# Performance work log

Hardware: AMD Instinct MI355X
Metric: run time of the kernel (lower is better)

## Reference

```python
import jax, jax.numpy as jnp
import numpy as np

N = 30000
E = 600000
IN = 64
HID = 128
EPS = 1e-5
HEADS_PER_LAYER = (4, 4, 1)


def _bn(x, g, b):
    # eval-mode BatchNorm: running_mean=0, running_var=1
    return x * (g / np.sqrt(1.0 + EPS)) + b


def _segment_softmax(e, dst, n):
    m = jax.ops.segment_max(e, dst, num_segments=n)
    ex = jnp.exp(e - m[dst])
    s = jax.ops.segment_sum(ex, dst, num_segments=n)
    return ex / (s[dst] + 1e-16)


def _gcn_conv(x, w, b, src, dst, norm, n):
    m = (x @ w)[src] * norm[:, None]            # [E+N, HID]
    return jax.ops.segment_sum(m, dst, num_segments=n) + b


def _gat_conv(x, w, a_src, a_dst, b, src, dst, n, heads):
    C = HID // heads
    xh = (x @ w).reshape(n, heads, C)
    asrc = (xh * a_src.reshape(heads, C)).sum(-1)   # [N, heads]
    adst = (xh * a_dst.reshape(heads, C)).sum(-1)
    e = jax.nn.leaky_relu(asrc[src] + adst[dst], 0.2)  # [E+N, heads]
    alpha = _segment_softmax(e, dst, n)
    out = jax.ops.segment_sum(xh[src] * alpha[:, :, None], dst, num_segments=n)
    return out.reshape(n, HID) + b


def _forward(x, gcn_in_w, gcn_in_b, gcn_res_w, gcn_res_b, gcn_w, gcn_b,
             gcn_bn_g, gcn_bn_b, gcn_c1w, gcn_c1b, gcn_c2w, gcn_c2b,
             gcn_c3w, gcn_c3b, gat_in_w, gat_in_b, gat_w, gat_asrc,
             gat_adst, gat_b, gat_bn_g, gat_bn_b, feat_imp, gat_c1w,
             gat_c1b, gat_cbn_g, gat_cbn_b, gat_c2w, gat_c2b, gat_c3w,
             gat_c3b, fin_w, fin_b, fin_bn_g, fin_bn_b, fin2_w, fin2_b,
             edge_index):
    n = x.shape[0]
    loop = jnp.arange(n, dtype=edge_index.dtype)
    src = jnp.concatenate([edge_index[0], loop])  # add self-loops
    dst = jnp.concatenate([edge_index[1], loop])
    # GCN symmetric normalization (with self-loops)
    deg = jax.ops.segment_sum(jnp.ones_like(dst, dtype=x.dtype), dst, num_segments=n)
    dis = jnp.where(deg > 0, jax.lax.rsqrt(jnp.maximum(deg, 1.0)), 0.0)
    norm = dis[src] * dis[dst]

    # ---- GCN branch (eval: dropout = identity, self-attn skipped since N>5000) ----
    xp = x @ gcn_in_w + gcn_in_b
    res = x @ gcn_res_w + gcn_res_b
    for i in range(3):
        xn = _gcn_conv(xp, gcn_w[i], gcn_b[i], src, dst, norm, n)
        xn = jax.nn.relu(_bn(xn, gcn_bn_g[i], gcn_bn_b[i]))
        if i % 2 == 1:
            xp = xn + res
            res = xp
        else:
            xp = xn
    h = jax.nn.relu(xp @ gcn_c1w + gcn_c1b)
    h = jax.nn.relu(h @ gcn_c2w + gcn_c2b)
    gcn_out = h @ gcn_c3w + gcn_c3b

    # ---- GAT branch ----
    xg = x @ gat_in_w + gat_in_b
    for i in range(3):
        xg = _gat_conv(xg, gat_w[i], gat_asrc[i], gat_adst[i], gat_b[i],
                       src, dst, n, HEADS_PER_LAYER[i])
        xg = jax.nn.elu(_bn(xg, gat_bn_g[i], gat_bn_b[i]))
    xg = xg * feat_imp
    h = jax.nn.relu(xg @ gat_c1w + gat_c1b)
    h = _bn(h, gat_cbn_g, gat_cbn_b)
    h = jax.nn.relu(h @ gat_c2w + gat_c2b)
    gat_out = h @ gat_c3w + gat_c3b

    # ---- fusion: N > 10000 -> weighted blend path ----
    fused = 0.6 * gcn_out + 0.4 * gat_out
    h = jax.nn.relu(fused @ fin_w + fin_b)
    h = _bn(h, fin_bn_g, fin_bn_b)
    return h @ fin2_w + fin2_b  # [N, 2]


def setup_inputs() -> dict:
    key = jax.random.key(0)
    ks = iter(jax.random.split(key, 64))

    def nrm(shape, scale=1.0):
        return jax.random.normal(next(ks), shape, dtype=jnp.float32) * scale

    s_in = 1.0 / np.sqrt(IN)
    s_h = 1.0 / np.sqrt(HID)
    inp = {}
    inp['x'] = nrm((N, IN))
    inp['edge_index'] = jax.random.randint(next(ks), (2, E), 0, N, dtype=jnp.int32)
    inp['gcn_in_w'] = nrm((IN, HID), s_in); inp['gcn_in_b'] = nrm((HID,), 0.01)
    inp['gcn_res_w'] = nrm((IN, HID), s_in); inp['gcn_res_b'] = nrm((HID,), 0.01)
    inp['gcn_w'] = nrm((3, HID, HID), s_h); inp['gcn_b'] = nrm((3, HID), 0.01)
    inp['gcn_bn_g'] = 1.0 + nrm((3, HID), 0.1); inp['gcn_bn_b'] = nrm((3, HID), 0.1)
    inp['gcn_c1w'] = nrm((HID, 64), s_h); inp['gcn_c1b'] = nrm((64,), 0.01)
    inp['gcn_c2w'] = nrm((64, 32), 0.125); inp['gcn_c2b'] = nrm((32,), 0.01)
    inp['gcn_c3w'] = nrm((32, HID), 0.18); inp['gcn_c3b'] = nrm((HID,), 0.01)
    inp['gat_in_w'] = nrm((IN, HID), s_in); inp['gat_in_b'] = nrm((HID,), 0.01)
    inp['gat_w'] = nrm((3, HID, HID), s_h)
    inp['gat_asrc'] = nrm((3, HID), s_h); inp['gat_adst'] = nrm((3, HID), s_h)
    inp['gat_b'] = nrm((3, HID), 0.01)
    inp['gat_bn_g'] = 1.0 + nrm((3, HID), 0.1); inp['gat_bn_b'] = nrm((3, HID), 0.1)
    inp['feat_imp'] = 1.0 + nrm((HID,), 0.1)
    inp['gat_c1w'] = nrm((HID, 64), s_h); inp['gat_c1b'] = nrm((64,), 0.01)
    inp['gat_cbn_g'] = 1.0 + nrm((64,), 0.1); inp['gat_cbn_b'] = nrm((64,), 0.1)
    inp['gat_c2w'] = nrm((64, 32), 0.125); inp['gat_c2b'] = nrm((32,), 0.01)
    inp['gat_c3w'] = nrm((32, HID), 0.18); inp['gat_c3b'] = nrm((HID,), 0.01)
    inp['fin_w'] = nrm((HID, 64), s_h); inp['fin_b'] = nrm((64,), 0.01)
    inp['fin_bn_g'] = 1.0 + nrm((64,), 0.1); inp['fin_bn_b'] = nrm((64,), 0.1)
    inp['fin2_w'] = nrm((64, 2), 0.125); inp['fin2_b'] = nrm((2,), 0.01)
    return inp


def reference(x, edge_index, gcn_in_w, gcn_in_b, gcn_res_w, gcn_res_b, gcn_w,
              gcn_b, gcn_bn_g, gcn_bn_b, gcn_c1w, gcn_c1b, gcn_c2w, gcn_c2b,
              gcn_c3w, gcn_c3b, gat_in_w, gat_in_b, gat_w, gat_asrc, gat_adst,
              gat_b, gat_bn_g, gat_bn_b, feat_imp, gat_c1w, gat_c1b, gat_cbn_g,
              gat_cbn_b, gat_c2w, gat_c2b, gat_c3w, gat_c3b, fin_w, fin_b,
              fin_bn_g, fin_bn_b, fin2_w, fin2_b):
    return _forward(x, gcn_in_w, gcn_in_b, gcn_res_w, gcn_res_b, gcn_w, gcn_b,
                    gcn_bn_g, gcn_bn_b, gcn_c1w, gcn_c1b, gcn_c2w, gcn_c2b,
                    gcn_c3w, gcn_c3b, gat_in_w, gat_in_b, gat_w, gat_asrc,
                    gat_adst, gat_b, gat_bn_g, gat_bn_b, feat_imp, gat_c1w,
                    gat_c1b, gat_cbn_g, gat_cbn_b, gat_c2w, gat_c2b, gat_c3w,
                    gat_c3b, fin_w, fin_b, fin_bn_g, fin_bn_b, fin2_w, fin2_b,
                    edge_index)
```

## Files before the change

kernel.cpp:

```cpp
#include <hip/hip_runtime.h>
#include <hip/hip_fp16.h>

#define RSQ_BN 0.9999950000374997f

typedef _Float16 f16x8 __attribute__((ext_vector_type(8)));
typedef float f32x4 __attribute__((ext_vector_type(4)));

union H8u { uint4 u4; __half h[8]; };
union H4u { uint2 u2; __half h[4]; };

__device__ __forceinline__ float leaky02(float x) { return x > 0.f ? x : 0.2f * x; }

__device__ __forceinline__ float4 ld4(const float* p) {
    return *reinterpret_cast<const float4*>(p);
}
__device__ __forceinline__ void ld8(float* d, const float* p) {
    float4 u = ld4(p), v = ld4(p + 4);
    d[0] = u.x; d[1] = u.y; d[2] = u.z; d[3] = u.w;
    d[4] = v.x; d[5] = v.y; d[6] = v.z; d[7] = v.w;
}


__global__ void hist_k(const int* __restrict__ edst, int* __restrict__ cnt, int E, int EN) {
    int i = blockIdx.x * 256 + threadIdx.x;
    if (i >= EN) return;
    int d = (i < E) ? edst[i] : (i - E);
    atomicAdd(&cnt[d], 1);
}

__global__ __launch_bounds__(256)
void scanA_k(const int* __restrict__ cnt, int* __restrict__ rowptr,
             int* __restrict__ bsum, int n) {
    __shared__ int sh[256];
    int t = threadIdx.x;
    int i = blockIdx.x * 256 + t;
    int v = (i < n) ? cnt[i] : 0;
    sh[t] = v;
    __syncthreads();
#pragma unroll
    for (int off = 1; off < 256; off <<= 1) {
        int u = 0;
        if (t >= off) u = sh[t - off];
        __syncthreads();
        sh[t] += u;
        __syncthreads();
    }
    if (i < n) rowptr[i] = sh[t] - v;
    if (t == 255) bsum[blockIdx.x] = sh[255];
}

__global__ __launch_bounds__(256)
void scanB_k(int* __restrict__ bsum, int nb) {
    __shared__ int sh[256];
    int t = threadIdx.x;
    int v = (t < nb) ? bsum[t] : 0;
    sh[t] = v;
    __syncthreads();
#pragma unroll
    for (int off = 1; off < 256; off <<= 1) {
        int u = 0;
        if (t >= off) u = sh[t - off];
        __syncthreads();
        sh[t] += u;
        __syncthreads();
    }
    if (t < nb) bsum[t] = sh[t] - v;
}

__global__ __launch_bounds__(256)
void scanC_k(const int* __restrict__ cnt, const int* __restrict__ bsum,
             int* __restrict__ rowptr, int* __restrict__ cursor,
             float* __restrict__ dis, int n, int EN) {
    int i = blockIdx.x * 256 + threadIdx.x;
    if (i < n) {
        int r = rowptr[i] + bsum[blockIdx.x];
        rowptr[i] = r;
        cursor[i] = r;
        dis[i] = rsqrtf((float)cnt[i]);
    }
    if (i == 0) rowptr[n] = EN;
}

__global__ void scatter_k(const int* __restrict__ esrc, const int* __restrict__ edst,
                          int* __restrict__ cursor, int* __restrict__ colidx, int E, int EN) {
    int i = blockIdx.x * 256 + threadIdx.x;
    if (i >= EN) return;
    int s, d;
    if (i < E) { s = esrc[i]; d = edst[i]; }
    else       { s = i - E; d = s; }
    int pos = atomicAdd(&cursor[d], 1);
    colidx[pos] = s;
}


__device__ __forceinline__ float pd0_elem(const float* __restrict__ gat_w,
                                          const float* __restrict__ gat_asrc,
                                          const float* __restrict__ gat_adst,
                                          int t, int col) {
    float p = 0.f;
    if (col < 4) {
        const float* w = gat_w + (size_t)t * 128 + col * 32;
        const float* av = gat_asrc + col * 32;
        for (int c2 = 0; c2 < 32; ++c2) p += w[c2] * av[c2];
    } else if (col >= 8 && col < 12) {
        int hh2 = col - 8;
        const float* w = gat_w + (size_t)t * 128 + hh2 * 32;
        const float* av = gat_adst + hh2 * 32;
        for (int c2 = 0; c2 < 32; ++c2) p += w[c2] * av[c2];
    }
    return p;
}

__global__ void wtx_all_k(const float* __restrict__ gcn_in_w, const float* __restrict__ gcn_res_w,
                          const float* __restrict__ gat_in_w,
                          const float* __restrict__ gcn_w, const float* __restrict__ gat_w,
                          const float* __restrict__ gcn_c1w, const float* __restrict__ gat_c1w,
                          const float* __restrict__ gcn_c3w, const float* __restrict__ gat_c3w,
                          const float* __restrict__ fin_w,
                          const float* __restrict__ gcn_c2w, const float* __restrict__ gat_c2w,
                          const float* __restrict__ gat_asrc, const float* __restrict__ gat_adst,
                          const float* __restrict__ gcn_in_b, const float* __restrict__ gat_in_b,
                          __half* __restrict__ WTin, __half* __restrict__ WTg,
                          __half* __restrict__ WTa, __half* __restrict__ WTc1,
                          __half* __restrict__ WTc3, __half* __restrict__ WTfin,
                          __half* __restrict__ WTc2, __half* __restrict__ WTd,
                          __half* __restrict__ Mg0, __half* __restrict__ Ma0,
                          __half* __restrict__ Da, float* __restrict__ cg0,
                          float* __restrict__ ca0, float* __restrict__ oa) {
    int idx = blockIdx.x * 256 + threadIdx.x;
    const float* src;
    __half* dst;
    int K, M, o;
    if (idx < 24576) {
        int mi = idx >> 13; o = idx & 8191;
        src = mi == 0 ? gcn_in_w : (mi == 1 ? gcn_res_w : gat_in_w);
        dst = WTin + mi * 8192; K = 64; M = 128;
    } else if (idx < 73728) {
        int r = idx - 24576; int mi = r >> 14; o = r & 16383;
        src = gcn_w + mi * 16384; dst = WTg + mi * 16384; K = 128; M = 128;
    } else if (idx < 122880) {
        int r = idx - 73728; int mi = r >> 14; o = r & 16383;
        src = gat_w + mi * 16384; dst = WTa + mi * 16384; K = 128; M = 128;
    } else if (idx < 139264) {
        int r = idx - 122880; int mi = r >> 13; o = r & 8191;
        src = mi ? gat_c1w : gcn_c1w; dst = WTc1 + mi * 8192; K = 128; M = 64;
    } else if (idx < 147456) {
        int r = idx - 139264; int mi = r >> 12; o = r & 4095;
        src = mi ? gat_c3w : gcn_c3w; dst = WTc3 + mi * 4096; K = 32; M = 128;
    } else if (idx < 155648) {
        o = idx - 147456; src = fin_w; dst = WTfin; K = 128; M = 64;
    } else if (idx < 159744) {
        int r = idx - 155648; int mi = r >> 11; o = r & 2047;
        src = mi ? gat_c2w : gcn_c2w; dst = WTc2 + mi * 2048; K = 64; M = 32;
    } else if (idx < 165888) {
        int r = idx - 159744;
        int layer = r >> 11; o = r & 2047;
        int j = o & 7, lane = (o >> 3) & 63, k32 = o >> 9;
        int col = lane & 15, quad = lane >> 4;
        int k = k32 * 32 + quad * 8 + j;
        int hh = (layer < 2) ? 4 : 1;
        int C = 128 / hh;
        float v = 0.f;
        if (col < hh) {
            const float* w = gat_w + (size_t)(layer * 128 + k) * 128 + col * C;
            const float* av = gat_asrc + layer * 128 + col * C;
            for (int c2 = 0; c2 < C; ++c2) v += w[c2] * av[c2];
        } else if (col >= 8 && col < 8 + hh) {
            int hthis = col - 8;
            const float* w = gat_w + (size_t)(layer * 128 + k) * 128 + hthis * C;
            const float* av = gat_adst + layer * 128 + hthis * C;
            for (int c2 = 0; c2 < C; ++c2) v += w[c2] * av[c2];
        }
        WTd[(size_t)layer * 2048 + o] = (__half)v;
        return;
    } else if (idx < 183296) {
        int r = idx - 165888;
        bool isA = r >= 8192;
        o = r & 8191;
        int j = o & 7, lane = (o >> 3) & 63, rr = o >> 9;
        int ct = rr >> 1, k32 = rr & 1;
        int m = lane & 15, quad = lane >> 4;
        int k = k32 * 32 + quad * 8 + j;
        int col = ct * 16 + m;
        const float* inw = isA ? gat_in_w : gcn_in_w;
        const float* lw  = isA ? gat_w : gcn_w;
        float v = 0.f;
        for (int t = 0; t < 128; ++t) v += inw[k * 128 + t] * lw[(size_t)t * 128 + col];
        (isA ? Ma0 : Mg0)[o] = (__half)v;
        return;
    } else if (idx < 184320) {
        o = idx - 183296;
        int j = o & 7, lane = (o >> 3) & 63, k32 = o >> 9;
        int col = lane & 15, quad = lane >> 4;
        int k = k32 * 32 + quad * 8 + j;
        float v = 0.f;
        if (col < 4 || (col >= 8 && col < 12)) {
            for (int t = 0; t < 128; ++t)
                v += gat_in_w[k * 128 + t] * pd0_elem(gat_w, gat_asrc, gat_adst, t, col);
        }
        Da[o] = (__half)v;
        return;
    } else if (idx < 184448) {
        int col = idx - 184320;
        float v = 0.f;
        for (int t = 0; t < 128; ++t) v += gcn_in_b[t] * gcn_w[(size_t)t * 128 + col];
        cg0[col] = v;
        return;
    } else if (idx < 184576) {
        int col = idx - 184448;
        float v = 0.f;
        for (int t = 0; t < 128; ++t) v += gat_in_b[t] * gat_w[(size_t)t * 128 + col];
        ca0[col] = v;
        return;
    } else if (idx < 184592) {
        int col = idx - 184576;
        float v = 0.f;
        if (col < 4 || (col >= 8 && col < 12)) {
            for (int t = 0; t < 128; ++t)
                v += gat_in_b[t] * pd0_elem(gat_w, gat_asrc, gat_adst, t, col);
        }
        oa[col] = v;
        return;
    } else return;
    int j = o & 7, lane = (o >> 3) & 63, r = o >> 9;
    int KD32 = K >> 5;
    int ct = r / KD32, k32 = r - ct * KD32;
    int m = lane & 15, quad = lane >> 4;
    int k = k32 * 32 + quad * 8 + j;
    int mcol = ct * 16 + m;
    dst[o] = (__half)src[k * M + mcol];
}


__device__ __forceinline__ f16x8 mk_af(const float* xr, int kb) {
    float4 v0 = ld4(xr + kb), v1 = ld4(xr + kb + 4);
    f16x8 af;
    af[0] = (_Float16)v0.x; af[1] = (_Float16)v0.y;
    af[2] = (_Float16)v0.z; af[3] = (_Float16)v0.w;
    af[4] = (_Float16)v1.x; af[5] = (_Float16)v1.y;
    af[6] = (_Float16)v1.z; af[7] = (_Float16)v1.w;
    return af;
}


__global__ __launch_bounds__(256)
void dual0_mfma_k(const float* __restrict__ X,
                  const __half* __restrict__ Mg0, const __half* __restrict__ Wres,
                  const float* __restrict__ resb,
                  const __half* __restrict__ Ma0, const __half* __restrict__ Da,
                  const float* __restrict__ cg0, const float* __restrict__ ca0,
                  const float* __restrict__ oa,
                  const float* __restrict__ dis,
                  __half* __restrict__ Yg, __half* __restrict__ Rout,
                  __half* __restrict__ Ya,
                  float* __restrict__ avp, float* __restrict__ bvp,
                  int hh, int n, int gper) {
    bool gat = blockIdx.x >= gper;
    int blk = gat ? blockIdx.x - gper : blockIdx.x;
    int wave = threadIdx.x >> 6, lane = threadIdx.x & 63;
    int m = lane & 15, quad = lane >> 4;
    int row0 = blk * 64 + wave * 16;
    int arow = min(row0 + m, n - 1);
    const float* xr = X + (size_t)arow * 64;
    f16x8 xf0 = mk_af(xr, quad * 8);
    f16x8 xf1 = mk_af(xr, 32 + quad * 8);
    int row = row0 + m;
    f32x4 acc[8];
    if (!gat) {
#pragma unroll
        for (int ct = 0; ct < 8; ++ct) acc[ct] = (f32x4){0.f, 0.f, 0.f, 0.f};
#pragma unroll
        for (int ct = 0; ct < 8; ++ct) {
            f16x8 b0 = *reinterpret_cast<const f16x8*>(Mg0 + ((ct * 2 + 0) << 9) + (lane << 3));
            f16x8 b1 = *reinterpret_cast<const f16x8*>(Mg0 + ((ct * 2 + 1) << 9) + (lane << 3));
            acc[ct] = __builtin_amdgcn_mfma_f32_16x16x32_f16(b0, xf0, acc[ct], 0, 0, 0);
            acc[ct] = __builtin_amdgcn_mfma_f32_16x16x32_f16(b1, xf1, acc[ct], 0, 0, 0);
        }
        if (row < n) {
            float dv = dis[row];
#pragma unroll
            for (int ct = 0; ct < 8; ++ct) {
                int col = ct * 16 + quad * 4;
                float4 cb = ld4(cg0 + col);
                H4u w;
                w.h[0] = (__half)((acc[ct][0] + cb.x) * dv);
                w.h[1] = (__half)((acc[ct][1] + cb.y) * dv);
                w.h[2] = (__half)((acc[ct][2] + cb.z) * dv);
                w.h[3] = (__half)((acc[ct][3] + cb.w) * dv);
                *reinterpret_cast<uint2*>(Yg + (size_t)row * 128 + col) = w.u2;
            }
        }
#pragma unroll
        for (int ct = 0; ct < 8; ++ct) acc[ct] = (f32x4){0.f, 0.f, 0.f, 0.f};
#pragma unroll
        for (int ct = 0; ct < 8; ++ct) {
            f16x8 b0 = *reinterpret_cast<const f16x8*>(Wres + ((ct * 2 + 0) << 9) + (lane << 3));
            f16x8 b1 = *reinterpret_cast<const f16x8*>(Wres + ((ct * 2 + 1) << 9) + (lane << 3));
            acc[ct] = __builtin_amdgcn_mfma_f32_16x16x32_f16(b0, xf0, acc[ct], 0, 0, 0);
            acc[ct] = __builtin_amdgcn_mfma_f32_16x16x32_f16(b1, xf1, acc[ct], 0, 0, 0);
        }
        if (row < n) {
#pragma unroll
            for (int ct = 0; ct < 8; ++ct) {
                int col = ct * 16 + quad * 4;
                float4 cb = ld4(resb + col);
                H4u w;
                w.h[0] = (__half)(acc[ct][0] + cb.x);
                w.h[1] = (__half)(acc[ct][1] + cb.y);
                w.h[2] = (__half)(acc[ct][2] + cb.z);
                w.h[3] = (__half)(acc[ct][3] + cb.w);
                *reinterpret_cast<uint2*>(Rout + (size_t)row * 128 + col) = w.u2;
            }
        }
    } else {
        f32x4 accd = (f32x4){0.f, 0.f, 0.f, 0.f};
#pragma unroll
        for (int ct = 0; ct < 8; ++ct) acc[ct] = (f32x4){0.f, 0.f, 0.f, 0.f};
#pragma unroll
        for (int ct = 0; ct < 8; ++ct) {
            f16x8 b0 = *reinterpret_cast<const f16x8*>(Ma0 + ((ct * 2 + 0) << 9) + (lane << 3));
            f16x8 b1 = *reinterpret_cast<const f16x8*>(Ma0 + ((ct * 2 + 1) << 9) + (lane << 3));
            acc[ct] = __builtin_amdgcn_mfma_f32_16x16x32_f16(b0, xf0, acc[ct], 0, 0, 0);
            acc[ct] = __builtin_amdgcn_mfma_f32_16x16x32_f16(b1, xf1, acc[ct], 0, 0, 0);
        }
        {
            f16x8 d0 = *reinterpret_cast<const f16x8*>(Da + (0 << 9) + (lane << 3));
            f16x8 d1 = *reinterpret_cast<const f16x8*>(Da + (1 << 9) + (lane << 3));
            accd = __builtin_amdgcn_mfma_f32_16x16x32_f16(d0, xf0, accd, 0, 0, 0);
            accd = __builtin_amdgcn_mfma_f32_16x16x32_f16(d1, xf1, accd, 0, 0, 0);
        }
        if (row < n) {
#pragma unroll
            for (int ct = 0; ct < 8; ++ct) {
                int col = ct * 16 + quad * 4;
                float4 cb = ld4(ca0 + col);
                H4u w;
                w.h[0] = (__half)(acc[ct][0] + cb.x);
                w.h[1] = (__half)(acc[ct][1] + cb.y);
                w.h[2] = (__half)(acc[ct][2] + cb.z);
                w.h[3] = (__half)(acc[ct][3] + cb.w);
                *reinterpret_cast<uint2*>(Ya + (size_t)row * 128 + col) = w.u2;
            }
            if (quad == 0) {
#pragma unroll
                for (int reg = 0; reg < 4; ++reg)
                    if (reg < hh) avp[row * hh + reg] = accd[reg] + oa[reg];
            } else if (quad == 2) {
#pragma unroll
                for (int reg = 0; reg < 4; ++reg)
                    if (reg < hh) bvp[row * hh + reg] = accd[reg] + oa[8 + reg];
            }
        }
    }
}


__global__ __launch_bounds__(256)
void dual128_mfma_k(const __half* __restrict__ Xg, const __half* __restrict__ WTg,
                    __half* __restrict__ Yg,
                    const __half* __restrict__ Xa, const __half* __restrict__ WTa,
                    __half* __restrict__ Ya,
                    const float* __restrict__ dis,
                    const __half* __restrict__ WTd,
                    float* __restrict__ avp, float* __restrict__ bvp,
                    int hh, int n, int gper) {
    bool gat = blockIdx.x >= gper;
    int blk = gat ? blockIdx.x - gper : blockIdx.x;
    const __half* X = gat ? Xa : Xg;
    const __half* WT = gat ? WTa : WTg;
    __half* Y = gat ? Ya : Yg;
    int wave = threadIdx.x >> 6;
    int lane = threadIdx.x & 63;
    int m = lane & 15, quad = lane >> 4;
    int row0 = blk * 64 + wave * 16;
    int arow = min(row0 + m, n - 1);
    const __half* xr = X + (size_t)arow * 128;
    f32x4 acc[8];
#pragma unroll
    for (int ct = 0; ct < 8; ++ct) acc[ct] = (f32x4){0.f, 0.f, 0.f, 0.f};
    int row = row0 + m;
    if (!gat) {
#pragma unroll
        for (int k32 = 0; k32 < 4; ++k32) {
            int kb = k32 * 32 + quad * 8;
            f16x8 af = *reinterpret_cast<const f16x8*>(xr + kb);
#pragma unroll
            for (int ct = 0; ct < 8; ++ct) {
                f16x8 bf = *reinterpret_cast<const f16x8*>(WT + ((ct * 4 + k32) << 9) + (lane << 3));
                acc[ct] = __builtin_amdgcn_mfma_f32_16x16x32_f16(bf, af, acc[ct], 0, 0, 0);
            }
        }
        if (row < n) {
            float dv = dis[row];
#pragma unroll
            for (int ct = 0; ct < 8; ++ct) {
                int col = ct * 16 + quad * 4;
                H4u w;
                w.h[0] = (__half)(acc[ct][0] * dv);
                w.h[1] = (__half)(acc[ct][1] * dv);
                w.h[2] = (__half)(acc[ct][2] * dv);
                w.h[3] = (__half)(acc[ct][3] * dv);
                *reinterpret_cast<uint2*>(Y + (size_t)row * 128 + col) = w.u2;
            }
        }
    } else {
        f32x4 accd = (f32x4){0.f, 0.f, 0.f, 0.f};
#pragma unroll
        for (int k32 = 0; k32 < 4; ++k32) {
            int kb = k32 * 32 + quad * 8;
            f16x8 af = *reinterpret_cast<const f16x8*>(xr + kb);
#pragma unroll
            for (int ct = 0; ct < 8; ++ct) {
                f16x8 bf = *reinterpret_cast<const f16x8*>(WT + ((ct * 4 + k32) << 9) + (lane << 3));
                acc[ct] = __builtin_amdgcn_mfma_f32_16x16x32_f16(bf, af, acc[ct], 0, 0, 0);
            }
            f16x8 bd = *reinterpret_cast<const f16x8*>(WTd + (k32 << 9) + (lane << 3));
            accd = __builtin_amdgcn_mfma_f32_16x16x32_f16(bd, af, accd, 0, 0, 0);
        }
        if (row < n) {
#pragma unroll
            for (int ct = 0; ct < 8; ++ct) {
                int col = ct * 16 + quad * 4;
                H4u w;
                w.h[0] = (__half)acc[ct][0];
                w.h[1] = (__half)acc[ct][1];
                w.h[2] = (__half)acc[ct][2];
                w.h[3] = (__half)acc[ct][3];
                *reinterpret_cast<uint2*>(Y + (size_t)row * 128 + col) = w.u2;
            }
            if (quad == 0) {
#pragma unroll
                for (int reg = 0; reg < 4; ++reg)
                    if (reg < hh) avp[row * hh + reg] = accd[reg];
            } else if (quad == 2) {
#pragma unroll
                for (int reg = 0; reg < 4; ++reg)
                    if (reg < hh) bvp[row * hh + reg] = accd[reg];
            }
        }
    }
}


__global__ __launch_bounds__(256)
void fused_gather_k(const int* __restrict__ rowptr, const int* __restrict__ colidx,
                    const float* __restrict__ dis,
                    const __half* __restrict__ Tg, const float* __restrict__ gbias,
                    const float* __restrict__ gbng, const float* __restrict__ gbnb,
                    const __half* __restrict__ res, __half* __restrict__ Yg,
                    const __half* __restrict__ Ta, const float* __restrict__ avp,
                    const float* __restrict__ bvp, const float* __restrict__ abias,
                    const float* __restrict__ abng, const float* __restrict__ abnb,
                    const float* __restrict__ fimp, __half* __restrict__ Ya,
                    int n, int hh, int log2C) {
    int idx = blockIdx.x * 256 + threadIdx.x;
    int i = idx >> 4;
    if (i >= n) return;
    int c = (idx & 15) * 8;
    int h = c >> log2C;
    float ad = bvp[i * hh + h];
    int p0 = rowptr[i], p1 = rowptr[i + 1];
    float g[8], a[8];
#pragma unroll
    for (int t = 0; t < 8; ++t) { g[t] = 0.f; a[t] = 0.f; }
    float m = -3.0e38f, s = 0.f;

    int ng = (p1 - p0 + 3) >> 2;
    int p = p0;
    int sx[4]; float av[4], vm[4];
#pragma unroll
    for (int j = 0; j < 4; ++j) {
        int q = p0 + j;
        vm[j] = (q < p1) ? 1.f : 0.f;
        sx[j] = colidx[min(q, p1 - 1)];
    }
#pragma unroll
    for (int j = 0; j < 4; ++j) av[j] = avp[sx[j] * hh + h];

    for (int gi = 0; gi < ng; ++gi) {
        uint4 qg[4], qa[4];
#pragma unroll
        for (int j = 0; j < 4; ++j)
            qg[j] = *reinterpret_cast<const uint4*>(Tg + (size_t)sx[j] * 128 + c);
#pragma unroll
        for (int j = 0; j < 4; ++j)
            qa[j] = *reinterpret_cast<const uint4*>(Ta + (size_t)sx[j] * 128 + c);
        int pn = p + 4;
        int sn[4]; float avn[4], vmn[4];
#pragma unroll
        for (int j = 0; j < 4; ++j) {
            int q = pn + j;
            vmn[j] = (q < p1) ? 1.f : 0.f;
            sn[j] = colidx[min(max(q, p0), p1 - 1)];
        }
#pragma unroll
        for (int j = 0; j < 4; ++j) avn[j] = avp[sn[j] * hh + h];
        float e0 = vm[0] > 0.f ? leaky02(av[0] + ad) : -3.0e38f;
        float e1 = vm[1] > 0.f ? leaky02(av[1] + ad) : -3.0e38f;
        float e2 = vm[2] > 0.f ? leaky02(av[2] + ad) : -3.0e38f;
        float e3 = vm[3] > 0.f ? leaky02(av[3] + ad) : -3.0e38f;
        float mc = fmaxf(fmaxf(e0, e1), fmaxf(e2, e3));
        float mn = fmaxf(m, mc);
        float scale = __expf(m - mn);
        float w0 = __expf(e0 - mn), w1 = __expf(e1 - mn);
        float w2 = __expf(e2 - mn), w3 = __expf(e3 - mn);
        s = s * scale + (w0 + w1 + w2 + w3);
        m = mn;
        {
            H8u k0, k1, k2, k3;
            k0.u4 = qg[0]; k1.u4 = qg[1]; k2.u4 = qg[2]; k3.u4 = qg[3];
#pragma unroll
            for (int t = 0; t < 8; ++t) {
                float v = g[t];
                v = fmaf(__half2float(k0.h[t]), vm[0], v);
                v = fmaf(__half2float(k1.h[t]), vm[1], v);
                v = fmaf(__half2float(k2.h[t]), vm[2], v);
                v = fmaf(__half2float(k3.h[t]), vm[3], v);
                g[t] = v;
            }
        }
        {
            H8u k0, k1, k2, k3;
            k0.u4 = qa[0]; k1.u4 = qa[1]; k2.u4 = qa[2]; k3.u4 = qa[3];
#pragma unroll
            for (int t = 0; t < 8; ++t) {
                float v = a[t] * scale;
                v = fmaf(__half2float(k0.h[t]), w0, v);
                v = fmaf(__half2float(k1.h[t]), w1, v);
                v = fmaf(__half2float(k2.h[t]), w2, v);
                v = fmaf(__half2float(k3.h[t]), w3, v);
                a[t] = v;
            }
        }
        p = pn;
#pragma unroll
        for (int j = 0; j < 4; ++j) { sx[j] = sn[j]; av[j] = avn[j]; vm[j] = vmn[j]; }
    }

    {
        float di = dis[i];
        float bb[8], gg[8], nb[8];
        ld8(bb, gbias + c); ld8(gg, gbng + c); ld8(nb, gbnb + c);
        float o[8];
#pragma unroll
        for (int t = 0; t < 8; ++t) {
            float v = g[t] * di + bb[t];
            o[t] = fmaxf(v * (gg[t] * RSQ_BN) + nb[t], 0.f);
        }
        if (res) {
            H8u rr;
            rr.u4 = *reinterpret_cast<const uint4*>(res + (size_t)i * 128 + c);
#pragma unroll
            for (int t = 0; t < 8; ++t) o[t] += __half2float(rr.h[t]);
        }
        H8u w;
#pragma unroll
        for (int t = 0; t < 8; ++t) w.h[t] = (__half)o[t];
        *reinterpret_cast<uint4*>(Yg + (size_t)i * 128 + c) = w.u4;
    }
    {
        float si = 1.f / (s + 1e-16f);
        float bb[8], gg[8], nb[8];
        ld8(bb, abias + c); ld8(gg, abng + c); ld8(nb, abnb + c);
        float o[8];
#pragma unroll
        for (int t = 0; t < 8; ++t) {
            float v = a[t] * si + bb[t];
            v = v * (gg[t] * RSQ_BN) + nb[t];
            o[t] = v > 0.f ? v : expm1f(v);
        }
        if (fimp) {
            float ff[8]; ld8(ff, fimp + c);
#pragma unroll
            for (int t = 0; t < 8; ++t) o[t] *= ff[t];
        }
        H8u w;
#pragma unroll
        for (int t = 0; t < 8; ++t) w.h[t] = (__half)o[t];
        *reinterpret_cast<uint4*>(Ya + (size_t)i * 128 + c) = w.u4;
    }
}


__global__ __launch_bounds__(256)
void fused_tail_k(const __half* __restrict__ Xg, const __half* __restrict__ Xa,
                  const __half* __restrict__ WTc1,
                  const float* __restrict__ c1bg, const float* __restrict__ c1ba,
                  const float* __restrict__ cbng, const float* __restrict__ cbnb,
                  const __half* __restrict__ WTc2,
                  const float* __restrict__ c2bg, const float* __restrict__ c2ba,
                  const __half* __restrict__ WTc3,
                  const float* __restrict__ c3bg, const float* __restrict__ c3ba,
                  const __half* __restrict__ WTfin, const float* __restrict__ finb,
                  const float* __restrict__ fbng, const float* __restrict__ fbnb,
                  const float* __restrict__ w2, const float* __restrict__ b2,
                  float* __restrict__ out, int n) {
    __shared__ alignas(16) __half h1s[2][64][88];
    __shared__ alignas(16) __half h2s[2][64][56];
    __shared__ alignas(16) __half Fs[64][152];
    int wave = threadIdx.x >> 6, lane = threadIdx.x & 63;
    int m = lane & 15, quad = lane >> 4;
    int row0 = blockIdx.x * 64 + wave * 16;
    int lr0 = wave * 16;
    int arow = min(row0 + m, n - 1);

#pragma unroll
    for (int br = 0; br < 2; ++br) {
        const __half* xr = (br ? Xa : Xg) + (size_t)arow * 128;
        const __half* WT = WTc1 + br * 8192;
        f32x4 acc[4];
#pragma unroll
        for (int ct = 0; ct < 4; ++ct) acc[ct] = (f32x4){0.f, 0.f, 0.f, 0.f};
#pragma unroll
        for (int k32 = 0; k32 < 4; ++k32) {
            int kb = k32 * 32 + quad * 8;
            f16x8 af = *reinterpret_cast<const f16x8*>(xr + kb);
#pragma unroll
            for (int ct = 0; ct < 4; ++ct) {
                f16x8 bf = *reinterpret_cast<const f16x8*>(WT + ((ct * 4 + k32) << 9) + (lane << 3));
                acc[ct] = __builtin_amdgcn_mfma_f32_16x16x32_f16(af, bf, acc[ct], 0, 0, 0);
            }
        }
        const float* bi = br ? c1ba : c1bg;
#pragma unroll
        for (int ct = 0; ct < 4; ++ct) {
            int col = ct * 16 + m;
            float cb = bi[col];
            float cg = br ? cbng[col] * RSQ_BN : 1.f;
            float cbb = br ? cbnb[col] : 0.f;
#pragma unroll
            for (int reg = 0; reg < 4; ++reg) {
                float v = fmaxf(acc[ct][reg] + cb, 0.f) * cg + cbb;
                h1s[br][lr0 + quad * 4 + reg][col] = (__half)v;
            }
        }
    }
    __syncthreads();
#pragma unroll
    for (int br = 0; br < 2; ++br) {
        f32x4 acc[2];
        acc[0] = (f32x4){0.f, 0.f, 0.f, 0.f};
        acc[1] = (f32x4){0.f, 0.f, 0.f, 0.f};
        const __half* WT = WTc2 + br * 2048;
#pragma unroll
        for (int k32 = 0; k32 < 2; ++k32) {
            int kb = k32 * 32 + quad * 8;
            f16x8 af = *reinterpret_cast<const f16x8*>(&h1s[br][lr0 + m][kb]);
#pragma unroll
            for (int ct = 0; ct < 2; ++ct) {
                f16x8 bf = *reinterpret_cast<const f16x8*>(WT + ((ct * 2 + k32) << 9) + (lane << 3));
                acc[ct] = __builtin_amdgcn_mfma_f32_16x16x32_f16(af, bf, acc[ct], 0, 0, 0);
            }
        }
        const float* bi = br ? c2ba : c2bg;
#pragma unroll
        for (int ct = 0; ct < 2; ++ct) {
            int col = ct * 16 + m;
            float cb = bi[col];
#pragma unroll
            for (int reg = 0; reg < 4; ++reg) {
                float v = fmaxf(acc[ct][reg] + cb, 0.f);
                h2s[br][lr0 + quad * 4 + reg][col] = (__half)v;
            }
        }
    }
    __syncthreads();
    {
        f32x4 ag[8], aa[8];
#pragma unroll
        for (int ct = 0; ct < 8; ++ct) {
            ag[ct] = (f32x4){0.f, 0.f, 0.f, 0.f};
            aa[ct] = (f32x4){0.f, 0.f, 0.f, 0.f};
        }
        int kb = quad * 8;
        f16x8 afg = *reinterpret_cast<const f16x8*>(&h2s[0][lr0 + m][kb]);
        f16x8 afa = *reinterpret_cast<const f16x8*>(&h2s[1][lr0 + m][kb]);
#pragma unroll
        for (int ct = 0; ct < 8; ++ct) {
            f16x8 bfg = *reinterpret_cast<const f16x8*>(WTc3 + (ct << 9) + (lane << 3));
            f16x8 bfa = *reinterpret_cast<const f16x8*>(WTc3 + 4096 + (ct << 9) + (lane << 3));
            ag[ct] = __builtin_amdgcn_mfma_f32_16x16x32_f16(afg, bfg, ag[ct], 0, 0, 0);
            aa[ct] = __builtin_amdgcn_mfma_f32_16x16x32_f16(afa, bfa, aa[ct], 0, 0, 0);
        }
#pragma unroll
        for (int ct = 0; ct < 8; ++ct) {
            int col = ct * 16 + m;
            float cb = 0.6f * c3bg[col] + 0.4f * c3ba[col];
#pragma unroll
            for (int reg = 0; reg < 4; ++reg) {
                float v = 0.6f * ag[ct][reg] + 0.4f * aa[ct][reg] + cb;
                Fs[lr0 + quad * 4 + reg][col] = (__half)v;
            }
        }
    }
    __syncthreads();
    {
        f32x4 acc[4];
#pragma unroll
        for (int ct = 0; ct < 4; ++ct) acc[ct] = (f32x4){0.f, 0.f, 0.f, 0.f};
#pragma unroll
        for (int k32 = 0; k32 < 4; ++k32) {
            int kb = k32 * 32 + quad * 8;
            f16x8 af = *reinterpret_cast<const f16x8*>(&Fs[lr0 + m][kb]);
#pragma unroll
            for (int ct = 0; ct < 4; ++ct) {
                f16x8 bf = *reinterpret_cast<const f16x8*>(WTfin + ((ct * 4 + k32) << 9) + (lane << 3));
                acc[ct] = __builtin_amdgcn_mfma_f32_16x16x32_f16(af, bf, acc[ct], 0, 0, 0);
            }
        }
        float p0[4] = {0.f, 0.f, 0.f, 0.f}, p1[4] = {0.f, 0.f, 0.f, 0.f};
#pragma unroll
        for (int ct = 0; ct < 4; ++ct) {
            int col = ct * 16 + m;
            float cb = finb[col];
            float cg = fbng[col] * RSQ_BN;
            float cbb = fbnb[col];
            float w20 = w2[2 * col], w21 = w2[2 * col + 1];
#pragma unroll
            for (int reg = 0; reg < 4; ++reg) {
                float v = fmaxf(acc[ct][reg] + cb, 0.f) * cg + cbb;
                p0[reg] += v * w20;
                p1[reg] += v * w21;
            }
        }
        for (int off = 1; off < 16; off <<= 1) {
#pragma unroll
            for (int reg = 0; reg < 4; ++reg) {
                p0[reg] += __shfl_xor(p0[reg], off);
                p1[reg] += __shfl_xor(p1[reg], off);
            }
        }
        if (m == 0) {
#pragma unroll
            for (int reg = 0; reg < 4; ++reg) {
                int row = row0 + quad * 4 + reg;
                if (row < n) {
                    out[row * 2] = p0[reg] + b2[0];
                    out[row * 2 + 1] = p1[reg] + b2[1];
                }
            }
        }
    }
}


static inline int cdiv(int a, int b) { return (a + b - 1) / b; }

extern "C" void kernel_launch(void* const* d_in, const int* in_sizes, int n_in,
                              void* d_out, int out_size, void* d_ws, size_t ws_size,
                              hipStream_t stream) {
    const float* x       = (const float*)d_in[0];
    const int*   ei      = (const int*)d_in[1];
    const float* gcn_in_w = (const float*)d_in[2];
    const float* gcn_in_b = (const float*)d_in[3];
    const float* gcn_res_w = (const float*)d_in[4];
    const float* gcn_res_b = (const float*)d_in[5];
    const float* gcn_w   = (const float*)d_in[6];
    const float* gcn_b   = (const float*)d_in[7];
    const float* gcn_bn_g = (const float*)d_in[8];
    const float* gcn_bn_b = (const float*)d_in[9];
    const float* gcn_c1w = (const float*)d_in[10];
    const float* gcn_c1b = (const float*)d_in[11];
    const float* gcn_c2w = (const float*)d_in[12];
    const float* gcn_c2b = (const float*)d_in[13];
    const float* gcn_c3w = (const float*)d_in[14];
    const float* gcn_c3b = (const float*)d_in[15];
    const float* gat_in_w = (const float*)d_in[16];
    const float* gat_in_b = (const float*)d_in[17];
    const float* gat_w   = (const float*)d_in[18];
    const float* gat_asrc = (const float*)d_in[19];
    const float* gat_adst = (const float*)d_in[20];
    const float* gat_b   = (const float*)d_in[21];
    const float* gat_bn_g = (const float*)d_in[22];
    const float* gat_bn_b = (const float*)d_in[23];
    const float* feat_imp = (const float*)d_in[24];
    const float* gat_c1w = (const float*)d_in[25];
    const float* gat_c1b = (const float*)d_in[26];
    const float* gat_cbn_g = (const float*)d_in[27];
    const float* gat_cbn_b = (const float*)d_in[28];
    const float* gat_c2w = (const float*)d_in[29];
    const float* gat_c2b = (const float*)d_in[30];
    const float* gat_c3w = (const float*)d_in[31];
    const float* gat_c3b = (const float*)d_in[32];
    const float* fin_w   = (const float*)d_in[33];
    const float* fin_b   = (const float*)d_in[34];
    const float* fin_bn_g = (const float*)d_in[35];
    const float* fin_bn_b = (const float*)d_in[36];
    const float* fin2_w  = (const float*)d_in[37];
    const float* fin2_b  = (const float*)d_in[38];

    const int N = in_sizes[0] / 64;
    const int E = in_sizes[1] / 2;
    const int EN = E + N;
    const int* esrc = ei;
    const int* edst = ei + E;

    char* wp = (char*)d_ws;
    auto alloc = [&](size_t bytes) -> void* {
        void* p = (void*)wp;
        wp += (bytes + 255) & ~(size_t)255;
        return p;
    };
    int* cnt    = (int*)alloc((size_t)N * 4);
    int* rowptr = (int*)alloc((size_t)(N + 1) * 4);
    int* cursor = (int*)alloc((size_t)N * 4);
    int* bsum   = (int*)alloc((size_t)256 * 4);
    int* colidx = (int*)alloc((size_t)EN * 4);
    float* dis  = (float*)alloc((size_t)N * 4);
    __half* A   = (__half*)alloc((size_t)N * 128 * 2);
    __half* B   = (__half*)alloc((size_t)N * 128 * 2);
    __half* G   = (__half*)alloc((size_t)N * 128 * 2);
    __half* H   = (__half*)alloc((size_t)N * 128 * 2);
    __half* R   = (__half*)alloc((size_t)N * 128 * 2);
    __half* Th1 = (__half*)alloc((size_t)N * 128 * 2);
    __half* Th2 = (__half*)alloc((size_t)N * 128 * 2);
    float* avv  = (float*)alloc((size_t)N * 4 * 4);
    float* bvv  = (float*)alloc((size_t)N * 4 * 4);
    __half* WTin = (__half*)alloc((size_t)3 * 8192 * 2);
    __half* WTg  = (__half*)alloc((size_t)3 * 16384 * 2);
    __half* WTa  = (__half*)alloc((size_t)3 * 16384 * 2);
    __half* WTc1 = (__half*)alloc((size_t)2 * 8192 * 2);
    __half* WTc3 = (__half*)alloc((size_t)2 * 4096 * 2);
    __half* WTfin = (__half*)alloc((size_t)8192 * 2);
    __half* WTc2 = (__half*)alloc((size_t)2 * 2048 * 2);
    __half* WTd  = (__half*)alloc((size_t)3 * 2048 * 2);
    __half* Mg0  = (__half*)alloc((size_t)8192 * 2);
    __half* Ma0  = (__half*)alloc((size_t)8192 * 2);
    __half* Da   = (__half*)alloc((size_t)1024 * 2);
    float* cg0   = (float*)alloc((size_t)128 * 4);
    float* ca0   = (float*)alloc((size_t)128 * 4);
    float* oa    = (float*)alloc((size_t)16 * 4);

    const int nScanB = cdiv(N, 256);
    hipMemsetAsync(cnt, 0, (size_t)N * 4, stream);
    hist_k<<<cdiv(EN, 256), 256, 0, stream>>>(edst, cnt, E, EN);
    scanA_k<<<nScanB, 256, 0, stream>>>(cnt, rowptr, bsum, N);
    scanB_k<<<1, 256, 0, stream>>>(bsum, nScanB);
    scanC_k<<<nScanB, 256, 0, stream>>>(cnt, bsum, rowptr, cursor, dis, N, EN);
    scatter_k<<<cdiv(EN, 256), 256, 0, stream>>>(esrc, edst, cursor, colidx, E, EN);
    wtx_all_k<<<721, 256, 0, stream>>>(gcn_in_w, gcn_res_w, gat_in_w, gcn_w, gat_w,
                                       gcn_c1w, gat_c1w, gcn_c3w, gat_c3w, fin_w,
                                       gcn_c2w, gat_c2w, gat_asrc, gat_adst,
                                       gcn_in_b, gat_in_b,
                                       WTin, WTg, WTa, WTc1, WTc3, WTfin, WTc2, WTd,
                                       Mg0, Ma0, Da, cg0, ca0, oa);

    const int g64r = cdiv(N, 64);
    const int gG   = cdiv(N, 16);

    dual0_mfma_k<<<2 * g64r, 256, 0, stream>>>(x, Mg0, WTin + 8192, gcn_res_b,
                                               Ma0, Da, cg0, ca0, oa, dis,
                                               Th1, R, Th2, avv, bvv, 4, N, g64r);
    fused_gather_k<<<gG, 256, 0, stream>>>(rowptr, colidx, dis,
                                           Th1, gcn_b, gcn_bn_g, gcn_bn_b, nullptr, A,
                                           Th2, avv, bvv, gat_b, gat_bn_g, gat_bn_b,
                                           nullptr, G, N, 4, 5);
    dual128_mfma_k<<<2 * g64r, 256, 0, stream>>>(A, WTg + 16384, Th1,
                                                 G, WTa + 16384, Th2, dis,
                                                 WTd + 2048, avv, bvv, 4, N, g64r);
    fused_gather_k<<<gG, 256, 0, stream>>>(rowptr, colidx, dis,
                                           Th1, gcn_b + 128, gcn_bn_g + 128, gcn_bn_b + 128,
                                           R, B,
                                           Th2, avv, bvv, gat_b + 128, gat_bn_g + 128,
                                           gat_bn_b + 128, nullptr, H, N, 4, 5);
    dual128_mfma_k<<<2 * g64r, 256, 0, stream>>>(B, WTg + 32768, Th1,
                                                 H, WTa + 32768, Th2, dis,
                                                 WTd + 4096, avv, bvv, 1, N, g64r);
    fused_gather_k<<<gG, 256, 0, stream>>>(rowptr, colidx, dis,
                                           Th1, gcn_b + 256, gcn_bn_g + 256, gcn_bn_b + 256,
                                           nullptr, A,
                                           Th2, avv, bvv, gat_b + 256, gat_bn_g + 256,
                                           gat_bn_b + 256, feat_imp, G, N, 1, 7);

    fused_tail_k<<<g64r, 256, 0, stream>>>(A, G,
                                           WTc1, gcn_c1b, gat_c1b, gat_cbn_g, gat_cbn_b,
                                           WTc2, gcn_c2b, gat_c2b,
                                           WTc3, gcn_c3b, gat_c3b,
                                           WTfin, fin_b, fin_bn_g, fin_bn_b,
                                           fin2_w, fin2_b, (float*)d_out, N);
}
```

Before: 435.7 us.

## Split fused gather threads across GCN/GAT tables and column halves

The fused gather kernel now assigns each thread a single table (GCN or GAT) and an 8-column chunk within one 64-column half, so each node is covered by two blocks with twice as many threads. Each thread keeps one accumulator array instead of two and issues half as many feature loads per edge. This halves per-thread register pressure and doubles the parallelism for latency hiding. In exchange, the colidx, rowptr and attention-score loads and the softmax arithmetic are repeated across more threads, and GCN threads perform redundant softmax work.

```diff
diff --git a/kernel.cpp b/kernel.cpp
--- a/kernel.cpp
+++ b/kernel.cpp
@@ -453,16 +453,19 @@
                     const float* __restrict__ abng, const float* __restrict__ abnb,
                     const float* __restrict__ fimp, __half* __restrict__ Ya,
                     int n, int hh, int log2C) {
-    int idx = blockIdx.x * 256 + threadIdx.x;
-    int i = idx >> 4;
+    int slice = blockIdx.x & 1;
+    int i = (blockIdx.x >> 1) * 16 + (threadIdx.x >> 4);
     if (i >= n) return;
-    int c = (idx & 15) * 8;
+    int k = threadIdx.x & 15;
+    int tbl = k >> 3;
+    int c = slice * 64 + (k & 7) * 8;
     int h = c >> log2C;
-    float ad = bvp[i * hh + h];
+    const __half* T = tbl ? Ta : Tg;
+    float ad = tbl ? bvp[i * hh + h] : 0.f;
     int p0 = rowptr[i], p1 = rowptr[i + 1];
-    float g[8], a[8];
-#pragma unroll
-    for (int t = 0; t < 8; ++t) { g[t] = 0.f; a[t] = 0.f; }
+    float acc[8];
+#pragma unroll
+    for (int t = 0; t < 8; ++t) acc[t] = 0.f;
     float m = -3.0e38f, s = 0.f;
 
     int ng = (p1 - p0 + 3) >> 2;
@@ -475,16 +478,13 @@
         sx[j] = colidx[min(q, p1 - 1)];
     }
 #pragma unroll
-    for (int j = 0; j < 4; ++j) av[j] = avp[sx[j] * hh + h];
+    for (int j = 0; j < 4; ++j) av[j] = tbl ? avp[sx[j] * hh + h] : 0.f;
 
     for (int gi = 0; gi < ng; ++gi) {
-        uint4 qg[4], qa[4];
+        uint4 q4[4];
 #pragma unroll
         for (int j = 0; j < 4; ++j)
-            qg[j] = *reinterpret_cast<const uint4*>(Tg + (size_t)sx[j] * 128 + c);
-#pragma unroll
-        for (int j = 0; j < 4; ++j)
-            qa[j] = *reinterpret_cast<const uint4*>(Ta + (size_t)sx[j] * 128 + c);
+            q4[j] = *reinterpret_cast<const uint4*>(T + (size_t)sx[j] * 128 + c);
         int pn = p + 4;
         int sn[4]; float avn[4], vmn[4];
 #pragma unroll
@@ -494,7 +494,7 @@
             sn[j] = colidx[min(max(q, p0), p1 - 1)];
         }
 #pragma unroll
-        for (int j = 0; j < 4; ++j) avn[j] = avp[sn[j] * hh + h];
+        for (int j = 0; j < 4; ++j) avn[j] = tbl ? avp[sn[j] * hh + h] : 0.f;
         float e0 = vm[0] > 0.f ? leaky02(av[0] + ad) : -3.0e38f;
         float e1 = vm[1] > 0.f ? leaky02(av[1] + ad) : -3.0e38f;
         float e2 = vm[2] > 0.f ? leaky02(av[2] + ad) : -3.0e38f;
@@ -506,45 +506,35 @@
         float w2 = __expf(e2 - mn), w3 = __expf(e3 - mn);
         s = s * scale + (w0 + w1 + w2 + w3);
         m = mn;
-        {
-            H8u k0, k1, k2, k3;
-            k0.u4 = qg[0]; k1.u4 = qg[1]; k2.u4 = qg[2]; k3.u4 = qg[3];
-#pragma unroll
-            for (int t = 0; t < 8; ++t) {
-                float v = g[t];
-                v = fmaf(__half2float(k0.h[t]), vm[0], v);
-                v = fmaf(__half2float(k1.h[t]), vm[1], v);
-                v = fmaf(__half2float(k2.h[t]), vm[2], v);
-                v = fmaf(__half2float(k3.h[t]), vm[3], v);
-                g[t] = v;
-            }
-        }
-        {
-            H8u k0, k1, k2, k3;
-            k0.u4 = qa[0]; k1.u4 = qa[1]; k2.u4 = qa[2]; k3.u4 = qa[3];
-#pragma unroll
-            for (int t = 0; t < 8; ++t) {
-                float v = a[t] * scale;
-                v = fmaf(__half2float(k0.h[t]), w0, v);
-                v = fmaf(__half2float(k1.h[t]), w1, v);
-                v = fmaf(__half2float(k2.h[t]), w2, v);
-                v = fmaf(__half2float(k3.h[t]), w3, v);
-                a[t] = v;
-            }
+        float u0 = tbl ? w0 : vm[0];
+        float u1 = tbl ? w1 : vm[1];
+        float u2 = tbl ? w2 : vm[2];
+        float u3 = tbl ? w3 : vm[3];
+        float sc = tbl ? scale : 1.f;
+        H8u k0, k1, k2, k3;
+        k0.u4 = q4[0]; k1.u4 = q4[1]; k2.u4 = q4[2]; k3.u4 = q4[3];
+#pragma unroll
+        for (int t = 0; t < 8; ++t) {
+            float v = acc[t] * sc;
+            v = fmaf(__half2float(k0.h[t]), u0, v);
+            v = fmaf(__half2float(k1.h[t]), u1, v);
+            v = fmaf(__half2float(k2.h[t]), u2, v);
+            v = fmaf(__half2float(k3.h[t]), u3, v);
+            acc[t] = v;
         }
         p = pn;
 #pragma unroll
         for (int j = 0; j < 4; ++j) { sx[j] = sn[j]; av[j] = avn[j]; vm[j] = vmn[j]; }
     }
 
-    {
+    if (tbl == 0) {
         float di = dis[i];
         float bb[8], gg[8], nb[8];
         ld8(bb, gbias + c); ld8(gg, gbng + c); ld8(nb, gbnb + c);
         float o[8];
 #pragma unroll
         for (int t = 0; t < 8; ++t) {
-            float v = g[t] * di + bb[t];
+            float v = acc[t] * di + bb[t];
             o[t] = fmaxf(v * (gg[t] * RSQ_BN) + nb[t], 0.f);
         }
         if (res) {
@@ -557,15 +547,14 @@
 #pragma unroll
         for (int t = 0; t < 8; ++t) w.h[t] = (__half)o[t];
         *reinterpret_cast<uint4*>(Yg + (size_t)i * 128 + c) = w.u4;
-    }
-    {
+    } else {
         float si = 1.f / (s + 1e-16f);
         float bb[8], gg[8], nb[8];
         ld8(bb, abias + c); ld8(gg, abng + c); ld8(nb, abnb + c);
         float o[8];
 #pragma unroll
         for (int t = 0; t < 8; ++t) {
-            float v = a[t] * si + bb[t];
+            float v = acc[t] * si + bb[t];
             v = v * (gg[t] * RSQ_BN) + nb[t];
             o[t] = v > 0.f ? v : expm1f(v);
         }
@@ -846,7 +835,7 @@
                                        Mg0, Ma0, Da, cg0, ca0, oa);
 
     const int g64r = cdiv(N, 64);
-    const int gG   = cdiv(N, 16);
+    const int gG   = 2 * cdiv(N, 16);
 
     dual0_mfma_k<<<2 * g64r, 256, 0, stream>>>(x, Mg0, WTin + 8192, gcn_res_b,
                                                Ma0, Da, cg0, ca0, oa, dis,
```

Result: slower. 444.9 us (+2.1%).

## Split fused gather into separate GCN and GAT block slices

Applied to the files above, without the earlier changes.

The fused gather kernel previously had each thread accumulate both the GCN sum and the GAT softmax-weighted sum for 8 channels. Now blocks are split four ways: two slices handle the GCN half-rows and two handle the GAT half-rows, each processing 32 nodes of 8 threads per block. This lowers per-thread register pressure and raises parallelism. In exchange, the colidx and index loads are repeated across slices, and the GAT softmax statistics are recomputed in both GAT slices. Column index loads also switch to nontemporal loads.

```diff
diff --git a/kernel.cpp b/kernel.cpp
--- a/kernel.cpp
+++ b/kernel.cpp
@@ -453,119 +453,134 @@
                     const float* __restrict__ abng, const float* __restrict__ abnb,
                     const float* __restrict__ fimp, __half* __restrict__ Ya,
                     int n, int hh, int log2C) {
-    int idx = blockIdx.x * 256 + threadIdx.x;
-    int i = idx >> 4;
+    int slice = blockIdx.x & 3;
+    int i = (blockIdx.x >> 2) * 32 + (threadIdx.x >> 3);
     if (i >= n) return;
-    int c = (idx & 15) * 8;
-    int h = c >> log2C;
-    float ad = bvp[i * hh + h];
+    int c = (slice & 1) * 64 + (threadIdx.x & 7) * 8;
     int p0 = rowptr[i], p1 = rowptr[i + 1];
-    float g[8], a[8];
-#pragma unroll
-    for (int t = 0; t < 8; ++t) { g[t] = 0.f; a[t] = 0.f; }
-    float m = -3.0e38f, s = 0.f;
-
     int ng = (p1 - p0 + 3) >> 2;
-    int p = p0;
-    int sx[4]; float av[4], vm[4];
-#pragma unroll
-    for (int j = 0; j < 4; ++j) {
-        int q = p0 + j;
-        vm[j] = (q < p1) ? 1.f : 0.f;
-        sx[j] = colidx[min(q, p1 - 1)];
-    }
-#pragma unroll
-    for (int j = 0; j < 4; ++j) av[j] = avp[sx[j] * hh + h];
-
-    for (int gi = 0; gi < ng; ++gi) {
-        uint4 qg[4], qa[4];
-#pragma unroll
-        for (int j = 0; j < 4; ++j)
-            qg[j] = *reinterpret_cast<const uint4*>(Tg + (size_t)sx[j] * 128 + c);
-#pragma unroll
-        for (int j = 0; j < 4; ++j)
-            qa[j] = *reinterpret_cast<const uint4*>(Ta + (size_t)sx[j] * 128 + c);
-        int pn = p + 4;
-        int sn[4]; float avn[4], vmn[4];
+    float acc[8];
+#pragma unroll
+    for (int t = 0; t < 8; ++t) acc[t] = 0.f;
+
+    if (slice < 2) {
+        int p = p0;
+        int sx[4]; float vm[4];
 #pragma unroll
         for (int j = 0; j < 4; ++j) {
-            int q = pn + j;
-            vmn[j] = (q < p1) ? 1.f : 0.f;
-            sn[j] = colidx[min(max(q, p0), p1 - 1)];
-        }
-#pragma unroll
-        for (int j = 0; j < 4; ++j) avn[j] = avp[sn[j] * hh + h];
-        float e0 = vm[0] > 0.f ? leaky02(av[0] + ad) : -3.0e38f;
-        float e1 = vm[1] > 0.f ? leaky02(av[1] + ad) : -3.0e38f;
-        float e2 = vm[2] > 0.f ? leaky02(av[2] + ad) : -3.0e38f;
-        float e3 = vm[3] > 0.f ? leaky02(av[3] + ad) : -3.0e38f;
-        float mc = fmaxf(fmaxf(e0, e1), fmaxf(e2, e3));
-        float mn = fmaxf(m, mc);
-        float scale = __expf(m - mn);
-        float w0 = __expf(e0 - mn), w1 = __expf(e1 - mn);
-        float w2 = __expf(e2 - mn), w3 = __expf(e3 - mn);
-        s = s * scale + (w0 + w1 + w2 + w3);
-        m = mn;
-        {
+            int q = p0 + j;
+            vm[j] = (q < p1) ? 1.f : 0.f;
+            sx[j] = __builtin_nontemporal_load(colidx + min(q, p1 - 1));
+        }
+        for (int gi = 0; gi < ng; ++gi) {
+            uint4 q4[4];
+#pragma unroll
+            for (int j = 0; j < 4; ++j)
+                q4[j] = *reinterpret_cast<const uint4*>(Tg + (size_t)sx[j] * 128 + c);
+            int pn = p + 4;
+            int sn[4]; float vmn[4];
+#pragma unroll
+            for (int j = 0; j < 4; ++j) {
+                int q = pn + j;
+                vmn[j] = (q < p1) ? 1.f : 0.f;
+                sn[j] = __builtin_nontemporal_load(colidx + min(max(q, p0), p1 - 1));
+            }
             H8u k0, k1, k2, k3;
-            k0.u4 = qg[0]; k1.u4 = qg[1]; k2.u4 = qg[2]; k3.u4 = qg[3];
+            k0.u4 = q4[0]; k1.u4 = q4[1]; k2.u4 = q4[2]; k3.u4 = q4[3];
 #pragma unroll
             for (int t = 0; t < 8; ++t) {
-                float v = g[t];
+                float v = acc[t];
                 v = fmaf(__half2float(k0.h[t]), vm[0], v);
                 v = fmaf(__half2float(k1.h[t]), vm[1], v);
                 v = fmaf(__half2float(k2.h[t]), vm[2], v);
                 v = fmaf(__half2float(k3.h[t]), vm[3], v);
-                g[t] = v;
-            }
-        }
-        {
+                acc[t] = v;
+            }
+            p = pn;
+#pragma unroll
+            for (int j = 0; j < 4; ++j) { sx[j] = sn[j]; vm[j] = vmn[j]; }
+        }
+        float di = dis[i];
+        float bb[8], gg[8], nb[8];
+        ld8(bb, gbias + c); ld8(gg, gbng + c); ld8(nb, gbnb + c);
+        float o[8];
+#pragma unroll
+        for (int t = 0; t < 8; ++t) {
+            float v = acc[t] * di + bb[t];
+            o[t] = fmaxf(v * (gg[t] * RSQ_BN) + nb[t], 0.f);
+        }
+        if (res) {
+            H8u rr;
+            rr.u4 = *reinterpret_cast<const uint4*>(res + (size_t)i * 128 + c);
+#pragma unroll
+            for (int t = 0; t < 8; ++t) o[t] += __half2float(rr.h[t]);
+        }
+        H8u w;
+#pragma unroll
+        for (int t = 0; t < 8; ++t) w.h[t] = (__half)o[t];
+        *reinterpret_cast<uint4*>(Yg + (size_t)i * 128 + c) = w.u4;
+    } else {
+        int h = c >> log2C;
+        float ad = bvp[i * hh + h];
+        float m = -3.0e38f, s = 0.f;
+        int p = p0;
+        int sx[4]; float av[4], vm[4];
+#pragma unroll
+        for (int j = 0; j < 4; ++j) {
+            int q = p0 + j;
+            vm[j] = (q < p1) ? 1.f : 0.f;
+            sx[j] = __builtin_nontemporal_load(colidx + min(q, p1 - 1));
+        }
+#pragma unroll
+        for (int j = 0; j < 4; ++j) av[j] = avp[sx[j] * hh + h];
+        for (int gi = 0; gi < ng; ++gi) {
+            uint4 q4[4];
+#pragma unroll
+            for (int j = 0; j < 4; ++j)
+                q4[j] = *reinterpret_cast<const uint4*>(Ta + (size_t)sx[j] * 128 + c);
+            int pn = p + 4;
+            int sn[4]; float avn[4], vmn[4];
+#pragma unroll
+            for (int j = 0; j < 4; ++j) {
+                int q = pn + j;
+                vmn[j] = (q < p1) ? 1.f : 0.f;
+                sn[j] = __builtin_nontemporal_load(colidx + min(max(q, p0), p1 - 1));
+            }
+#pragma unroll
+            for (int j = 0; j < 4; ++j) avn[j] = avp[sn[j] * hh + h];
+            float e0 = vm[0] > 0.f ? leaky02(av[0] + ad) : -3.0e38f;
+            float e1 = vm[1] > 0.f ? leaky02(av[1] + ad) : -3.0e38f;
+            float e2 = vm[2] > 0.f ? leaky02(av[2] + ad) : -3.0e38f;
+            float e3 = vm[3] > 0.f ? leaky02(av[3] + ad) : -3.0e38f;
+            float mc = fmaxf(fmaxf(e0, e1), fmaxf(e2, e3));
+            float mn = fmaxf(m, mc);
+            float scale = __expf(m - mn);
+            float w0 = __expf(e0 - mn), w1 = __expf(e1 - mn);
+            float w2 = __expf(e2 - mn), w3 = __expf(e3 - mn);
+            s = s * scale + (w0 + w1 + w2 + w3);
+            m = mn;
             H8u k0, k1, k2, k3;
-            k0.u4 = qa[0]; k1.u4 = qa[1]; k2.u4 = qa[2]; k3.u4 = qa[3];
+            k0.u4 = q4[0]; k1.u4 = q4[1]; k2.u4 = q4[2]; k3.u4 = q4[3];
 #pragma unroll
             for (int t = 0; t < 8; ++t) {
-                float v = a[t] * scale;
+                float v = acc[t] * scale;
                 v = fmaf(__half2float(k0.h[t]), w0, v);
                 v = fmaf(__half2float(k1.h[t]), w1, v);
                 v = fmaf(__half2float(k2.h[t]), w2, v);
                 v = fmaf(__half2float(k3.h[t]), w3, v);
-                a[t] = v;
-            }
-        }
-        p = pn;
-#pragma unroll
-        for (int j = 0; j < 4; ++j) { sx[j] = sn[j]; av[j] = avn[j]; vm[j] = vmn[j]; }
-    }
-
-    {
-        float di = dis[i];
-        float bb[8], gg[8], nb[8];
-        ld8(bb, gbias + c); ld8(gg, gbng + c); ld8(nb, gbnb + c);
-        float o[8];
-#pragma unroll
-        for (int t = 0; t < 8; ++t) {
-            float v = g[t] * di + bb[t];
-            o[t] = fmaxf(v * (gg[t] * RSQ_BN) + nb[t], 0.f);
-        }
-        if (res) {
-            H8u rr;
-            rr.u4 = *reinterpret_cast<const uint4*>(res + (size_t)i * 128 + c);
-#pragma unroll
-            for (int t = 0; t < 8; ++t) o[t] += __half2float(rr.h[t]);
-        }
-        H8u w;
-#pragma unroll
-        for (int t = 0; t < 8; ++t) w.h[t] = (__half)o[t];
-        *reinterpret_cast<uint4*>(Yg + (size_t)i * 128 + c) = w.u4;
-    }
-    {
+                acc[t] = v;
+            }
+            p = pn;
+#pragma unroll
+            for (int j = 0; j < 4; ++j) { sx[j] = sn[j]; av[j] = avn[j]; vm[j] = vmn[j]; }
+        }
         float si = 1.f / (s + 1e-16f);
         float bb[8], gg[8], nb[8];
         ld8(bb, abias + c); ld8(gg, abng + c); ld8(nb, abnb + c);
         float o[8];
 #pragma unroll
         for (int t = 0; t < 8; ++t) {
-            float v = a[t] * si + bb[t];
+            float v = acc[t] * si + bb[t];
             v = v * (gg[t] * RSQ_BN) + nb[t];
             o[t] = v > 0.f ? v : expm1f(v);
         }
@@ -846,7 +861,7 @@
                                        Mg0, Ma0, Da, cg0, ca0, oa);
 
     const int g64r = cdiv(N, 64);
-    const int gG   = cdiv(N, 16);
+    const int gG   = 4 * cdiv(N, 32);
 
     dual0_mfma_k<<<2 * g64r, 256, 0, stream>>>(x, Mg0, WTin + 8192, gcn_res_b,
                                                Ma0, Da, cg0, ca0, oa, dis,
```

Result: slower. 495.4 us (+13.7%).
